# Kernel optimization log

Measured on AMD Instinct MI355X. Metric: run time of the kernel, lower is better.

## Reference

```python
import jax, jax.numpy as jnp
import numpy as np
from jax import lax

BS, T, D, H, FF, KS, L = 8, 1024, 512, 8, 2048, 5, 6
DK = D // H  # 64


def setup_inputs() -> dict:
    key = jax.random.key(0)
    ks_ = jax.random.split(key, 16)
    n = lambda i, shape, s=0.02: jax.random.normal(ks_[i], shape, jnp.float32) * s
    return dict(
        q_embed_data=n(0, (BS, T, D), 1.0),
        qa_embed_data=n(1, (BS, T, D), 1.0),
        pid_embed_data=n(2, (BS, T, T), 1.0),  # unused for emb_type='qid'
        conv_w=n(3, (D, D, KS)), conv_b=jnp.zeros((D,), jnp.float32),
        sqrt_beta=n(4, (1, 1, D), 1.0),
        sm_g=jnp.ones((D,), jnp.float32), sm_b=jnp.zeros((D,), jnp.float32),
        k_w=n(5, (L, D, D)), k_b=jnp.zeros((L, D), jnp.float32),
        v_w=n(6, (L, D, D)), v_b=jnp.zeros((L, D), jnp.float32),
        out_w=n(7, (L, D, D)), out_b=jnp.zeros((L, D), jnp.float32),
        gammas=n(8, (L, H, 1, 1), 0.1),
        ln1_g=jnp.ones((L, D), jnp.float32), ln1_b=jnp.zeros((L, D), jnp.float32),
        ff1_w=n(9, (L, D, FF)), ff1_b=jnp.zeros((L, FF), jnp.float32),
        ff2_w=n(10, (L, FF, D)), ff2_b=jnp.zeros((L, D), jnp.float32),
        ln2_g=jnp.ones((L, D), jnp.float32), ln2_b=jnp.zeros((L, D), jnp.float32),
    )


def _layernorm(x, g, b, eps):
    m = jnp.mean(x, axis=-1, keepdims=True)
    v = jnp.mean((x - m) ** 2, axis=-1, keepdims=True)
    return g * (x - m) / jnp.sqrt(v + eps) + b


def _smooth(x, conv_w, conv_b, sqrt_beta, g, b):
    # x: [B,T,D]. Causal Conv1d: left-pad KS-1, crop to length T.
    xt = jnp.transpose(x, (0, 2, 1))  # [B,D,T]
    trend = lax.conv_general_dilated(
        xt, conv_w, window_strides=(1,), padding=[(KS - 1, 0)],
        dimension_numbers=('NCH', 'OIH', 'NCH')) + conv_b[None, :, None]
    trend = jnp.transpose(trend, (0, 2, 1))  # [B,T,D]
    random = x - trend
    seq = trend + sqrt_beta ** 2 * random
    return _layernorm(seq + x, g, b, 1e-12)


def _decay_attention(q, k, v, mask, gamma_param, zero_pad):
    # q,k,v: [B,H,T,DK]; mask: [1,1,T,T] bool
    neg = jnp.float32(-1e32)
    scores = jnp.einsum('bhqd,bhkd->bhqk', q, k) / np.float32(np.sqrt(DK))
    # detached distance-effect computation (no_grad in torch)
    s_ = jax.nn.softmax(jnp.where(mask, scores, neg), axis=-1) * mask.astype(jnp.float32)
    distcum = jnp.cumsum(s_, axis=-1)
    disttot = jnp.sum(s_, axis=-1, keepdims=True)
    idx = jnp.arange(T, dtype=jnp.float32)
    pos = jnp.abs(idx[None, :] - idx[:, None])[None, None]  # |j - i|
    dist = jnp.sqrt(jnp.clip((disttot - distcum) * pos, 0.0, None))
    dist = lax.stop_gradient(dist)
    gamma = -jax.nn.softplus(gamma_param)[None]  # [1,H,1,1]
    total_effect = jnp.clip(jnp.exp(dist * gamma), 1e-5, 1e5)
    scores = jnp.where(mask, scores * total_effect, neg)
    scores = jax.nn.softmax(scores, axis=-1)
    if zero_pad:
        scores = scores.at[:, :, 0, :].set(0.0)
    return jnp.einsum('bhqk,bhkd->bhqd', scores, v)


def _tlayer(p, i, mtype, q_in, k_in, v_in, apply_pos, masks):
    mask = masks[mtype]
    def heads(x, W, b):
        return jnp.transpose((x @ W + b).reshape(BS, T, H, DK), (0, 2, 1, 3))
    # kq_same=True: q and k both use k_linear
    q = heads(q_in, p['k_w'][i], p['k_b'][i])
    k = heads(k_in, p['k_w'][i], p['k_b'][i])
    v = heads(v_in, p['v_w'][i], p['v_b'][i])
    out = _decay_attention(q, k, v, mask, p['gammas'][i], zero_pad=(mtype == 0))
    concat = jnp.transpose(out, (0, 2, 1, 3)).reshape(BS, T, D)
    q2 = concat @ p['out_w'][i] + p['out_b'][i]
    x = _layernorm(q_in + q2, p['ln1_g'][i], p['ln1_b'][i], 1e-5)
    if apply_pos:
        hdn = jax.nn.relu(x @ p['ff1_w'][i] + p['ff1_b'][i])
        x = _layernorm(x + hdn @ p['ff2_w'][i] + p['ff2_b'][i],
                       p['ln2_g'][i], p['ln2_b'][i], 1e-5)
    return x


def _forward(q_embed_data, qa_embed_data, pid_embed_data,
             conv_w, conv_b, sqrt_beta, sm_g, sm_b,
             k_w, k_b, v_w, v_b, out_w, out_b, gammas,
             ln1_g, ln1_b, ff1_w, ff1_b, ff2_w, ff2_b, ln2_g, ln2_b):
    p = dict(k_w=k_w, k_b=k_b, v_w=v_w, v_b=v_b, out_w=out_w, out_b=out_b,
             gammas=gammas, ln1_g=ln1_g, ln1_b=ln1_b, ff1_w=ff1_w, ff1_b=ff1_b,
             ff2_w=ff2_w, ff2_b=ff2_b, ln2_g=ln2_g, ln2_b=ln2_b)
    tri = jnp.tril(jnp.ones((T, T), bool))
    masks = {1: tri[None, None], 0: jnp.tril(jnp.ones((T, T), bool), -1)[None, None]}
    x = _smooth(q_embed_data, conv_w, conv_b, sqrt_beta, sm_g, sm_b)
    y = _smooth(qa_embed_data, conv_w, conv_b, sqrt_beta, sm_g, sm_b)
    # blocks_1: n_blocks=2 layers, mask=1, self-attn on y
    y = _tlayer(p, 0, 1, y, y, y, True, masks)
    y = _tlayer(p, 1, 1, y, y, y, True, masks)
    # blocks_2: 4 layers alternating (mask=1, no FFN) / (mask=0, values=y, FFN)
    x = _tlayer(p, 2, 1, x, x, x, False, masks)
    x = _tlayer(p, 3, 0, x, x, y, True, masks)
    x = _tlayer(p, 4, 1, x, x, x, False, masks)
    x = _tlayer(p, 5, 0, x, x, y, True, masks)
    return x


def reference(q_embed_data, qa_embed_data, pid_embed_data,
              conv_w, conv_b, sqrt_beta, sm_g, sm_b,
              k_w, k_b, v_w, v_b, out_w, out_b, gammas,
              ln1_g, ln1_b, ff1_w, ff1_b, ff2_w, ff2_b, ln2_g, ln2_b):
    return _forward(q_embed_data, qa_embed_data, pid_embed_data,
                    conv_w, conv_b, sqrt_beta, sm_g, sm_b,
                    k_w, k_b, v_w, v_b, out_w, out_b, gammas,
                    ln1_g, ln1_b, ff1_w, ff1_b, ff2_w, ff2_b, ln2_g, ln2_b)
```

## Files before the change

### kernel.cpp

```cpp
#include <hip/hip_runtime.h>
#include <math.h>

#define T_  1024
#define D_  512
#define H_  8
#define DK_ 64
#define FF_ 2048
#define BSZ 8
#define M_  (BSZ * T_)
#define TP_ (T_ + 4)

typedef unsigned short u16;
typedef unsigned int u32;
typedef __attribute__((ext_vector_type(8))) __bf16 bf16x8;
typedef __attribute__((ext_vector_type(4))) float f32x4;

__device__ __forceinline__ u16 f2bf(float f) {
    unsigned int u = __float_as_uint(f);
    u += 0x7fffu + ((u >> 16) & 1u);
    return (u16)(u >> 16);
}
__device__ __forceinline__ float bf2f(u16 b) {
    return __uint_as_float((unsigned int)b << 16);
}

__device__ __forceinline__ void gload16(const void* g, void* l) {
    __builtin_amdgcn_global_load_lds(
        (const __attribute__((address_space(1))) void*)g,
        (__attribute__((address_space(3))) void*)l, 16, 0, 0);
}

__global__ void __launch_bounds__(256) gemm_mfma(
    const u16* __restrict__ A, const u16* __restrict__ Bt,
    const float* __restrict__ bias, void* __restrict__ Cout,
    int N, int K, int mode)
{
    __shared__ __align__(16) u16 As[128 * 32];
    __shared__ __align__(16) u16 Bs[128 * 32];
    int tid = threadIdx.x;
    int wid = tid >> 6, lane = tid & 63;
    int quad = lane >> 4, mrow = lane & 15;
    int m0 = blockIdx.y * 128, n0 = blockIdx.x * 128;
    int wr = (wid >> 1) * 64, wc = (wid & 1) * 64;

    const u16* Ap = A + (size_t)(m0 + (tid >> 2)) * K + (tid & 3) * 8;
    const u16* Bp = Bt + (size_t)(n0 + (tid >> 2)) * K + (tid & 3) * 8;
    char* lA = (char*)As + wid * 1024;
    char* lB = (char*)Bs + wid * 1024;

    f32x4 acc[4][4] = {};
    for (int k0 = 0; k0 < K; k0 += 32) {
        __syncthreads();
        gload16(Ap + k0, lA);
        gload16(Ap + (size_t)64 * K + k0, lA + 4096);
        gload16(Bp + k0, lB);
        gload16(Bp + (size_t)64 * K + k0, lB + 4096);
        asm volatile("s_waitcnt vmcnt(0)" ::: "memory");
        __syncthreads();
        bf16x8 af[4], bf[4];
#pragma unroll
        for (int t = 0; t < 4; ++t) {
            af[t] = *(const bf16x8*)&As[(wr + t * 16 + mrow) * 32 + quad * 8];
            bf[t] = *(const bf16x8*)&Bs[(wc + t * 16 + mrow) * 32 + quad * 8];
        }
#pragma unroll
        for (int rt = 0; rt < 4; ++rt)
#pragma unroll
            for (int ct = 0; ct < 4; ++ct)
                acc[rt][ct] = __builtin_amdgcn_mfma_f32_16x16x32_bf16(
                    af[rt], bf[ct], acc[rt][ct], 0, 0, 0);
    }

#pragma unroll
    for (int ct = 0; ct < 4; ++ct) {
        int col = n0 + wc + ct * 16 + mrow;
        float bv = bias ? bias[col] : 0.f;
#pragma unroll
        for (int rt = 0; rt < 4; ++rt) {
            int rowb = m0 + wr + rt * 16 + quad * 4;
            if (mode == 0) {
                float* C = (float*)Cout;
#pragma unroll
                for (int e = 0; e < 4; ++e)
                    C[(size_t)(rowb + e) * N + col] = acc[rt][ct][e] + bv;
            } else if (mode == 1) {
                u16* C = (u16*)Cout;
#pragma unroll
                for (int e = 0; e < 4; ++e)
                    C[(size_t)(rowb + e) * N + col] = f2bf(fmaxf(acc[rt][ct][e] + bv, 0.f));
            } else {
                u16* C = (u16*)Cout;
#pragma unroll
                for (int e = 0; e < 4; ++e)
                    C[(size_t)(rowb + e) * N + col] = f2bf(acc[rt][ct][e] + bv);
            }
        }
    }
}

__global__ void __launch_bounds__(256) gemm64_mfma(
    const u16* __restrict__ A, const u16* __restrict__ Bt,
    const float* __restrict__ bias, void* __restrict__ Cout,
    int N, int K, int mode)
{
    __shared__ __align__(16) u16 As[64 * 32];
    __shared__ __align__(16) u16 Bs[64 * 32];
    int tid = threadIdx.x;
    int wid = tid >> 6, lane = tid & 63;
    int quad = lane >> 4, mrow = lane & 15;
    int m0 = blockIdx.y * 64, n0 = blockIdx.x * 64;
    int wc = wid * 16;

    const u16* Ap = A + (size_t)(m0 + (tid >> 2)) * K + (tid & 3) * 8;
    const u16* Bp = Bt + (size_t)(n0 + (tid >> 2)) * K + (tid & 3) * 8;
    char* lA = (char*)As + wid * 1024;
    char* lB = (char*)Bs + wid * 1024;

    f32x4 acc[4] = {};
    for (int k0 = 0; k0 < K; k0 += 32) {
        __syncthreads();
        gload16(Ap + k0, lA);
        gload16(Bp + k0, lB);
        asm volatile("s_waitcnt vmcnt(0)" ::: "memory");
        __syncthreads();
        bf16x8 af[4];
#pragma unroll
        for (int t = 0; t < 4; ++t)
            af[t] = *(const bf16x8*)&As[(t * 16 + mrow) * 32 + quad * 8];
        bf16x8 bf = *(const bf16x8*)&Bs[(wc + mrow) * 32 + quad * 8];
#pragma unroll
        for (int rt = 0; rt < 4; ++rt)
            acc[rt] = __builtin_amdgcn_mfma_f32_16x16x32_bf16(af[rt], bf, acc[rt], 0, 0, 0);
    }

    int col = n0 + wc + mrow;
    float bv = bias ? bias[col] : 0.f;
#pragma unroll
    for (int rt = 0; rt < 4; ++rt) {
        int rowb = m0 + rt * 16 + quad * 4;
        if (mode == 0) {
            float* C = (float*)Cout;
#pragma unroll
            for (int e = 0; e < 4; ++e)
                C[(size_t)(rowb + e) * N + col] = acc[rt][e] + bv;
        } else if (mode == 1) {
            u16* C = (u16*)Cout;
#pragma unroll
            for (int e = 0; e < 4; ++e)
                C[(size_t)(rowb + e) * N + col] = f2bf(fmaxf(acc[rt][e] + bv, 0.f));
        } else if (mode == 2) {
            u16* C = (u16*)Cout;
#pragma unroll
            for (int e = 0; e < 4; ++e)
                C[(size_t)(rowb + e) * N + col] = f2bf(acc[rt][e] + bv);
        } else {
            u16* C = (u16*)Cout;
            int h = col >> 6, dl = col & 63;
#pragma unroll
            for (int e = 0; e < 4; ++e) {
                int row = rowb + e;
                int b = row >> 10, t = row & (T_ - 1);
                C[(((size_t)(b * H_ + h) * DK_ + dl) << 10) + t] =
                    f2bf(acc[rt][e] + bv);
            }
        }
    }
}

__global__ void __launch_bounds__(256) conv64_mfma(
    const u16* __restrict__ Xp, const u16* __restrict__ W5t, float* __restrict__ C)
{
    __shared__ __align__(16) u16 As[64 * 32];
    __shared__ __align__(16) u16 Bs[64 * 32];
    int tid = threadIdx.x;
    int wid = tid >> 6, lane = tid & 63;
    int quad = lane >> 4, mrow = lane & 15;
    int m0 = blockIdx.y * 64, n0 = blockIdx.x * 64;
    int wc = wid * 16;
    int b = m0 >> 10, tloc = m0 & (T_ - 1);

    const u16* Ap0 = Xp + (size_t)(b * TP_ + tloc + (tid >> 2)) * D_ + (tid & 3) * 8;
    const u16* Bp0 = W5t + (size_t)(n0 + (tid >> 2)) * D_ + (tid & 3) * 8;
    char* lA = (char*)As + wid * 1024;
    char* lB = (char*)Bs + wid * 1024;

    f32x4 acc[4] = {};
    for (int ks = 0; ks < 5; ++ks) {
        const u16* Ap = Ap0 + ks * D_;
        const u16* Bp = Bp0 + (size_t)ks * D_ * D_;
        for (int k0 = 0; k0 < D_; k0 += 32) {
            __syncthreads();
            gload16(Ap + k0, lA);
            gload16(Bp + k0, lB);
            asm volatile("s_waitcnt vmcnt(0)" ::: "memory");
            __syncthreads();
            bf16x8 af[4];
#pragma unroll
            for (int t = 0; t < 4; ++t)
                af[t] = *(const bf16x8*)&As[(t * 16 + mrow) * 32 + quad * 8];
            bf16x8 bf = *(const bf16x8*)&Bs[(wc + mrow) * 32 + quad * 8];
#pragma unroll
            for (int rt = 0; rt < 4; ++rt)
                acc[rt] = __builtin_amdgcn_mfma_f32_16x16x32_bf16(af[rt], bf, acc[rt], 0, 0, 0);
        }
    }
    int col = n0 + wc + mrow;
#pragma unroll
    for (int rt = 0; rt < 4; ++rt) {
        int row = m0 + rt * 16 + quad * 4;
#pragma unroll
        for (int e = 0; e < 4; ++e)
            C[(size_t)(row + e) * D_ + col] = acc[rt][e];
    }
}

__global__ void __launch_bounds__(256) qk_mfma(
    const u16* __restrict__ Qh, u16* __restrict__ S)
{
    int kt = blockIdx.x, it = blockIdx.y;
    if (kt > it) return;
    int z = blockIdx.z;
    int b = z >> 3, h = z & 7;
    __shared__ __align__(16) u16 As[64 * 32];
    __shared__ __align__(16) u16 Bs[64 * 32];
    int tid = threadIdx.x;
    int wid = tid >> 6, lane = tid & 63;
    int quad = lane >> 4, mrow = lane & 15;
    int wc = wid * 16;

    const u16* Ap = Qh + (size_t)(b * T_ + it * 64 + (tid >> 2)) * D_ + h * DK_ + (tid & 3) * 8;
    const u16* Bp = Qh + (size_t)(b * T_ + kt * 64 + (tid >> 2)) * D_ + h * DK_ + (tid & 3) * 8;
    char* lA = (char*)As + wid * 1024;
    char* lB = (char*)Bs + wid * 1024;

    f32x4 acc[4] = {};
#pragma unroll
    for (int k0 = 0; k0 < DK_; k0 += 32) {
        __syncthreads();
        gload16(Ap + k0, lA);
        gload16(Bp + k0, lB);
        asm volatile("s_waitcnt vmcnt(0)" ::: "memory");
        __syncthreads();
        bf16x8 af[4];
#pragma unroll
        for (int t = 0; t < 4; ++t)
            af[t] = *(const bf16x8*)&As[(t * 16 + mrow) * 32 + quad * 8];
        bf16x8 bf = *(const bf16x8*)&Bs[(wc + mrow) * 32 + quad * 8];
#pragma unroll
        for (int rt = 0; rt < 4; ++rt)
            acc[rt] = __builtin_amdgcn_mfma_f32_16x16x32_bf16(af[rt], bf, acc[rt], 0, 0, 0);
    }
    int col = kt * 64 + wc + mrow;
#pragma unroll
    for (int rt = 0; rt < 4; ++rt) {
        int row = it * 64 + rt * 16 + quad * 4;
#pragma unroll
        for (int e = 0; e < 4; ++e)
            S[((size_t)z * T_ + row + e) * T_ + col] = f2bf(acc[rt][e] * 0.125f);
    }
}

#define LOG2E 1.4426950408889634f

#define DPPF(OLDB, X, CTRL, RM) \
    __uint_as_float((u32)__builtin_amdgcn_update_dpp( \
        (int)(OLDB), __float_as_int(X), CTRL, RM, 0xf, false))

__device__ __forceinline__ float scan_add_f(float x) {
    x += DPPF(0u, x, 0x111, 0xf);
    x += DPPF(0u, x, 0x112, 0xf);
    x += DPPF(0u, x, 0x114, 0xf);
    x += DPPF(0u, x, 0x118, 0xf);
    x += DPPF(0u, x, 0x142, 0xa);
    x += DPPF(0u, x, 0x143, 0xc);
    return x;
}
__device__ __forceinline__ float scan_max_f(float x) {
    x = fmaxf(x, DPPF(0xff800000u, x, 0x111, 0xf));
    x = fmaxf(x, DPPF(0xff800000u, x, 0x112, 0xf));
    x = fmaxf(x, DPPF(0xff800000u, x, 0x114, 0xf));
    x = fmaxf(x, DPPF(0xff800000u, x, 0x118, 0xf));
    x = fmaxf(x, DPPF(0xff800000u, x, 0x142, 0xa));
    x = fmaxf(x, DPPF(0xff800000u, x, 0x143, 0xc));
    return x;
}
__device__ __forceinline__ float lane63(float x) {
    return __uint_as_float((u32)__builtin_amdgcn_readlane(__float_as_int(x), 63));
}

__global__ void __launch_bounds__(256) decay_rows(
    u16* __restrict__ S, const float* __restrict__ gam_l, int mtype)
{
    int tid = threadIdx.x;
    int wv = tid >> 6, lane = tid & 63;
    int i = blockIdx.x * 4 + wv;
    int z = blockIdx.y;
    int h = z & 7;
    u16* row = S + ((size_t)z * T_ + i) * T_;
    int kmax = (mtype == 0) ? (i - 1) : i;

    if (kmax < 0) {
        row[lane] = 0;
        return;
    }
    int nc    = (kmax >> 7) + 1;
    int nfull = (kmax + 1) >> 7;
    int wend  = (((i >> 6) + 1) * 64 + 127) >> 7;

    float s0[8], s1[8], p0[8], p1[8];
    int base = lane * 2;

    float mx = -1e30f;
#pragma unroll
    for (int c = 0; c < 8; ++c) {
        if (c >= nc) break;
        int k = c * 128 + base;
        u32 v = *(const u32*)(row + k);
        float a = __uint_as_float(v << 16) * LOG2E;
        float b = __uint_as_float(v & 0xffff0000u) * LOG2E;
        if (c >= nfull) {
            a = (k     <= kmax) ? a : -1.5e30f;
            b = (k + 1 <= kmax) ? b : -1.5e30f;
        }
        s0[c] = a; s1[c] = b;
        mx = fmaxf(mx, fmaxf(a, b));
    }
    mx = lane63(scan_max_f(mx));

    float t1 = 0.f;
#pragma unroll
    for (int c = 0; c < 8; ++c) {
        if (c >= nc) break;
        float e0 = __builtin_amdgcn_exp2f(s0[c] - mx);
        float e1 = __builtin_amdgcn_exp2f(s1[c] - mx);
        p0[c] = e0; p1[c] = e1;
        t1 += e0 + e1;
    }
    float tot = lane63(scan_add_f(t1));
    float inv1 = 1.f / tot;

    float gam = -log1pf(__expf(gam_l[h])) * LOG2E;
    float fi = (float)i;
    float kf = (float)base;
    float running = 0.f;
#pragma unroll
    for (int c = 0; c < 8; ++c) {
        if (c >= nc) break;
        float sc = scan_add_f(p0[c] + p1[c]);
        float incl1 = running + sc;
        float incl0 = incl1 - p1[c];
        running += lane63(sc);
        float rem0 = fmaxf((tot - incl0) * inv1, 0.f);
        float rem1 = fmaxf((tot - incl1) * inv1, 0.f);
        float pos0 = fabsf(kf - fi);
        float pos1 = fabsf(kf + 1.f - fi);
        float ef0 = __builtin_amdgcn_fmed3f(
            __builtin_amdgcn_exp2f(sqrtf(rem0 * pos0) * gam), 1e-5f, 1e5f);
        float ef1 = __builtin_amdgcn_fmed3f(
            __builtin_amdgcn_exp2f(sqrtf(rem1 * pos1) * gam), 1e-5f, 1e5f);
        s0[c] *= ef0;
        s1[c] *= ef1;
        kf += 128.f;
    }

    float mx2 = -1e30f;
#pragma unroll
    for (int c = 0; c < 8; ++c) {
        if (c >= nc) break;
        mx2 = fmaxf(mx2, fmaxf(s0[c], s1[c]));
    }
    mx2 = lane63(scan_max_f(mx2));
    float t2 = 0.f;
#pragma unroll
    for (int c = 0; c < 8; ++c) {
        if (c >= nc) break;
        float e0 = __builtin_amdgcn_exp2f(s0[c] - mx2);
        float e1 = __builtin_amdgcn_exp2f(s1[c] - mx2);
        p0[c] = e0; p1[c] = e1;
        t2 += e0 + e1;
    }
    float tot2 = lane63(scan_add_f(t2));
    float inv2 = 1.f / tot2;

#pragma unroll
    for (int c = 0; c < 8; ++c) {
        if (c >= nc) break;
        float lo = p0[c] * inv2, hi = p1[c] * inv2;
        u32 o;
        asm("v_cvt_pk_bf16_f32 %0, %1, %2" : "=v"(o) : "v"(lo), "v"(hi));
        *(u32*)(row + c * 128 + base) = o;
    }
#pragma unroll
    for (int c = 0; c < 8; ++c) {
        if (c < nc) continue;
        if (c >= wend) break;
        *(u32*)(row + c * 128 + base) = 0u;
    }
}

__global__ void __launch_bounds__(256) pv_mfma(
    const u16* __restrict__ P, const u16* __restrict__ Vt,
    u16* __restrict__ O)
{
    int mt = blockIdx.x;
    int z = blockIdx.y;
    int b = z >> 3, h = z & 7;
    __shared__ __align__(16) u16 As[64 * 32];
    __shared__ __align__(16) u16 Bs[64 * 32];
    int tid = threadIdx.x;
    int wid = tid >> 6, lane = tid & 63;
    int quad = lane >> 4, mrow = lane & 15;
    int wc = wid * 16;

    const u16* Ap = P + ((size_t)z * T_ + mt * 64 + (tid >> 2)) * T_ + (tid & 3) * 8;
    const u16* Bp = Vt + ((size_t)z * DK_ + (tid >> 2)) * T_ + (tid & 3) * 8;
    char* lA = (char*)As + wid * 1024;
    char* lB = (char*)Bs + wid * 1024;

    int kend = (mt + 1) * 64;
    f32x4 acc[4] = {};
    for (int k0 = 0; k0 < kend; k0 += 32) {
        __syncthreads();
        gload16(Ap + k0, lA);
        gload16(Bp + k0, lB);
        asm volatile("s_waitcnt vmcnt(0)" ::: "memory");
        __syncthreads();
        bf16x8 af[4];
#pragma unroll
        for (int t = 0; t < 4; ++t)
            af[t] = *(const bf16x8*)&As[(t * 16 + mrow) * 32 + quad * 8];
        bf16x8 bf = *(const bf16x8*)&Bs[(wc + mrow) * 32 + quad * 8];
#pragma unroll
        for (int rt = 0; rt < 4; ++rt)
            acc[rt] = __builtin_amdgcn_mfma_f32_16x16x32_bf16(af[rt], bf, acc[rt], 0, 0, 0);
    }
    int col = h * DK_ + wc + mrow;
#pragma unroll
    for (int rt = 0; rt < 4; ++rt) {
        int row = b * T_ + mt * 64 + rt * 16 + quad * 4;
#pragma unroll
        for (int e = 0; e < 4; ++e)
            O[(size_t)(row + e) * D_ + col] = f2bf(acc[rt][e]);
    }
}

__global__ void __launch_bounds__(256) transpose_bf16(
    const float* __restrict__ W, u16* __restrict__ Wt, int K, int N)
{
    __shared__ float tile[32][33];
    size_t base = (size_t)blockIdx.z * K * N;
    W += base; Wt += base;
    int k0 = blockIdx.y * 32, n0 = blockIdx.x * 32;
    int r = threadIdx.x >> 3, c = (threadIdx.x & 7) * 4;
    float4 v = *(const float4*)(W + (size_t)(k0 + r) * N + n0 + c);
    tile[r][c] = v.x; tile[r][c + 1] = v.y; tile[r][c + 2] = v.z; tile[r][c + 3] = v.w;
    __syncthreads();
    ushort4 o;
    o.x = f2bf(tile[c + 0][r]); o.y = f2bf(tile[c + 1][r]);
    o.z = f2bf(tile[c + 2][r]); o.w = f2bf(tile[c + 3][r]);
    *(ushort4*)(Wt + (size_t)(n0 + r) * K + k0 + c) = o;
}

__global__ void w5_gather(const float* __restrict__ cw, u16* __restrict__ W5t)
{
    int idx = blockIdx.x * 256 + threadIdx.x;
    if (idx >= 5 * D_ * D_) return;
    int ks = idx / (D_ * D_);
    int rem = idx - ks * (D_ * D_);
    int o = rem >> 9, i = rem & (D_ - 1);
    W5t[idx] = f2bf(cw[((size_t)o * D_ + i) * 5 + ks]);
}

__global__ void cast_pad(const float* __restrict__ x, const float* __restrict__ y,
                         u16* __restrict__ Xp, u16* __restrict__ Yp)
{
    int idx = blockIdx.x * 256 + threadIdx.x;
    if (idx >= BSZ * TP_ * D_) return;
    int d = idx & (D_ - 1);
    int rowp = idx >> 9;
    int b = rowp / TP_;
    int t = rowp - b * TP_;
    u16 vx = 0, vy = 0;
    if (t >= 4) {
        size_t src = ((size_t)(b * T_ + t - 4) << 9) + d;
        vx = f2bf(x[src]); vy = f2bf(y[src]);
    }
    Xp[idx] = vx; Yp[idx] = vy;
}

__global__ void __launch_bounds__(256) smooth_ln(
    const float* __restrict__ x, const float* __restrict__ trend,
    const float* __restrict__ conv_b, const float* __restrict__ sqrt_beta,
    const float* __restrict__ g, const float* __restrict__ bb,
    float* __restrict__ out, u16* __restrict__ outb)
{
    __shared__ float s_red[8];
    int row = blockIdx.x, tid = threadIdx.x;
    int lane = tid & 63, wid = tid >> 6;
    float2 xv = ((const float2*)(x + (size_t)row * D_))[tid];
    float2 tv = ((const float2*)(trend + (size_t)row * D_))[tid];
    float2 cb = ((const float2*)conv_b)[tid];
    float2 sb = ((const float2*)sqrt_beta)[tid];
    float t0 = tv.x + cb.x, t1 = tv.y + cb.y;
    float v0 = t0 + sb.x * sb.x * (xv.x - t0) + xv.x;
    float v1 = t1 + sb.y * sb.y * (xv.y - t1) + xv.y;
    float s = v0 + v1, sq = v0 * v0 + v1 * v1;
    for (int o = 32; o > 0; o >>= 1) { s += __shfl_xor(s, o, 64); sq += __shfl_xor(sq, o, 64); }
    if (lane == 0) { s_red[wid] = s; s_red[4 + wid] = sq; }
    __syncthreads();
    s = s_red[0] + s_red[1] + s_red[2] + s_red[3];
    sq = s_red[4] + s_red[5] + s_red[6] + s_red[7];
    float mean = s * (1.f / D_);
    float var = sq * (1.f / D_) - mean * mean;
    if (var < 0.f) var = 0.f;
    float rstd = rsqrtf(var + 1e-12f);
    float2 gv = ((const float2*)g)[tid];
    float2 bv = ((const float2*)bb)[tid];
    float2 o2;
    o2.x = gv.x * (v0 - mean) * rstd + bv.x;
    o2.y = gv.y * (v1 - mean) * rstd + bv.y;
    ((float2*)(out + (size_t)row * D_))[tid] = o2;
    ushort2 ob; ob.x = f2bf(o2.x); ob.y = f2bf(o2.y);
    ((ushort2*)(outb + (size_t)row * D_))[tid] = ob;
}

__global__ void __launch_bounds__(256) add_ln(
    const float* __restrict__ a, const float* __restrict__ c,
    const float* __restrict__ g, const float* __restrict__ bb,
    float* __restrict__ out, u16* __restrict__ outb, float eps)
{
    __shared__ float s_red[8];
    int row = blockIdx.x, tid = threadIdx.x;
    int lane = tid & 63, wid = tid >> 6;
    float2 av = ((const float2*)(a + (size_t)row * D_))[tid];
    float2 cv = ((const float2*)(c + (size_t)row * D_))[tid];
    float v0 = av.x + cv.x;
    float v1 = av.y + cv.y;
    float s = v0 + v1, sq = v0 * v0 + v1 * v1;
    for (int o = 32; o > 0; o >>= 1) { s += __shfl_xor(s, o, 64); sq += __shfl_xor(sq, o, 64); }
    if (lane == 0) { s_red[wid] = s; s_red[4 + wid] = sq; }
    __syncthreads();
    s = s_red[0] + s_red[1] + s_red[2] + s_red[3];
    sq = s_red[4] + s_red[5] + s_red[6] + s_red[7];
    float mean = s * (1.f / D_);
    float var = sq * (1.f / D_) - mean * mean;
    if (var < 0.f) var = 0.f;
    float rstd = rsqrtf(var + eps);
    float2 gv = ((const float2*)g)[tid];
    float2 bv = ((const float2*)bb)[tid];
    float2 o2;
    o2.x = gv.x * (v0 - mean) * rstd + bv.x;
    o2.y = gv.y * (v1 - mean) * rstd + bv.y;
    ((float2*)(out + (size_t)row * D_))[tid] = o2;
    ushort2 ob; ob.x = f2bf(o2.x); ob.y = f2bf(o2.y);
    ((ushort2*)(outb + (size_t)row * D_))[tid] = ob;
}

extern "C" void kernel_launch(void* const* d_in, const int* in_sizes, int n_in,
                              void* d_out, int out_size, void* d_ws, size_t ws_size,
                              hipStream_t stream)
{
    const float* q_embed   = (const float*)d_in[0];
    const float* qa_embed  = (const float*)d_in[1];
    const float* conv_w    = (const float*)d_in[3];
    const float* conv_b    = (const float*)d_in[4];
    const float* sqrt_beta = (const float*)d_in[5];
    const float* sm_g      = (const float*)d_in[6];
    const float* sm_b      = (const float*)d_in[7];
    const float* k_w       = (const float*)d_in[8];
    const float* k_b       = (const float*)d_in[9];
    const float* v_w       = (const float*)d_in[10];
    const float* v_b       = (const float*)d_in[11];
    const float* out_w     = (const float*)d_in[12];
    const float* out_b     = (const float*)d_in[13];
    const float* gammas    = (const float*)d_in[14];
    const float* ln1_g     = (const float*)d_in[15];
    const float* ln1_b     = (const float*)d_in[16];
    const float* ff1_w     = (const float*)d_in[17];
    const float* ff1_b     = (const float*)d_in[18];
    const float* ff2_w     = (const float*)d_in[19];
    const float* ff2_b     = (const float*)d_in[20];
    const float* ln2_g     = (const float*)d_in[21];
    const float* ln2_b     = (const float*)d_in[22];

    const size_t NT = (size_t)M_ * D_;
    float* X = (float*)d_out;
    char* w = (char*)d_ws;
    float* Y  = (float*)w; w += NT * 4;
    float* Fb = (float*)w; w += NT * 4;
    u16* Sb = (u16*)w;
    u16* Hb = Sb;
    u16* Xpad = Sb;
    u16* Ypad = Xpad + (size_t)BSZ * TP_ * D_;
    u16* W5t  = Ypad + (size_t)BSZ * TP_ * D_;
    w += (size_t)BSZ * H_ * T_ * T_ * 2;
    u16* Xb  = (u16*)w; w += NT * 2;
    u16* Yb  = (u16*)w; w += NT * 2;
    u16* Cb  = (u16*)w; w += NT * 2;
    u16* Qh  = (u16*)w; w += NT * 2;
    u16* Vt  = (u16*)w; w += NT * 2;
    u16* KWt = (u16*)w; w += (size_t)6 * D_ * D_ * 2;
    u16* VWt = (u16*)w; w += (size_t)6 * D_ * D_ * 2;
    u16* OWt = (u16*)w; w += (size_t)6 * D_ * D_ * 2;
    u16* F1t = (u16*)w; w += (size_t)6 * D_ * FF_ * 2;
    u16* F2t = (u16*)w; w += (size_t)6 * FF_ * D_ * 2;

    dim3 blk(256);

    cast_pad<<<(BSZ * TP_ * D_ + 255) / 256, blk, 0, stream>>>(q_embed, qa_embed, Xpad, Ypad);
    w5_gather<<<(5 * D_ * D_ + 255) / 256, blk, 0, stream>>>(conv_w, W5t);
    transpose_bf16<<<dim3(D_ / 32, D_ / 32, 6), blk, 0, stream>>>(k_w, KWt, D_, D_);
    transpose_bf16<<<dim3(D_ / 32, D_ / 32, 6), blk, 0, stream>>>(v_w, VWt, D_, D_);
    transpose_bf16<<<dim3(D_ / 32, D_ / 32, 6), blk, 0, stream>>>(out_w, OWt, D_, D_);
    transpose_bf16<<<dim3(FF_ / 32, D_ / 32, 6), blk, 0, stream>>>(ff1_w, F1t, D_, FF_);
    transpose_bf16<<<dim3(D_ / 32, FF_ / 32, 6), blk, 0, stream>>>(ff2_w, F2t, FF_, D_);

    conv64_mfma<<<dim3(8, 128), blk, 0, stream>>>(Xpad, W5t, Fb);
    smooth_ln<<<M_, blk, 0, stream>>>(q_embed, Fb, conv_b, sqrt_beta, sm_g, sm_b, X, Xb);
    conv64_mfma<<<dim3(8, 128), blk, 0, stream>>>(Ypad, W5t, Fb);
    smooth_ln<<<M_, blk, 0, stream>>>(qa_embed, Fb, conv_b, sqrt_beta, sm_g, sm_b, Y, Yb);

    auto layer = [&](int l, int mtype, float* io, u16* iob, const u16* vinb, bool ffn) {
        gemm64_mfma<<<dim3(8, 128), blk, 0, stream>>>(iob, KWt + (size_t)l * D_ * D_,
                                                      k_b + (size_t)l * D_, Qh, D_, D_, 2);
        gemm64_mfma<<<dim3(8, 128), blk, 0, stream>>>(vinb, VWt + (size_t)l * D_ * D_,
                                                      v_b + (size_t)l * D_, Vt, D_, D_, 3);
        qk_mfma<<<dim3(16, 16, 64), blk, 0, stream>>>(Qh, Sb);
        decay_rows<<<dim3(T_ / 4, 64), blk, 0, stream>>>(Sb, gammas + l * H_, mtype);
        pv_mfma<<<dim3(16, 64), blk, 0, stream>>>(Sb, Vt, Cb);
        gemm64_mfma<<<dim3(8, 128), blk, 0, stream>>>(Cb, OWt + (size_t)l * D_ * D_,
                                                      out_b + (size_t)l * D_, Fb, D_, D_, 0);
        add_ln<<<M_, blk, 0, stream>>>(io, Fb, ln1_g + l * D_, ln1_b + l * D_, io, iob, 1e-5f);
        if (ffn) {
            gemm_mfma<<<dim3(16, 64), blk, 0, stream>>>(iob, F1t + (size_t)l * D_ * FF_,
                                                        ff1_b + (size_t)l * FF_, Hb, FF_, D_, 1);
            gemm64_mfma<<<dim3(8, 128), blk, 0, stream>>>(Hb, F2t + (size_t)l * FF_ * D_,
                                                          ff2_b + (size_t)l * D_, Fb, D_, FF_, 0);
            add_ln<<<M_, blk, 0, stream>>>(io, Fb, ln2_g + l * D_, ln2_b + l * D_, io, iob, 1e-5f);
        }
    };

    layer(0, 1, Y, Yb, Yb, true);
    layer(1, 1, Y, Yb, Yb, true);
    layer(2, 1, X, Xb, Xb, false);
    layer(3, 0, X, Xb, Yb, true);
    layer(4, 1, X, Xb, Xb, false);
    layer(5, 0, X, Xb, Yb, true);
}
```

Measured before the change: 1.804 ms.

## Double-buffer LDS tiles in all MFMA GEMM kernels to overlap loads

```diff
diff --git a/kernel.cpp b/kernel.cpp
--- a/kernel.cpp
+++ b/kernel.cpp
@@ -35,8 +35,8 @@
     const float* __restrict__ bias, void* __restrict__ Cout,
     int N, int K, int mode)
 {
-    __shared__ __align__(16) u16 As[128 * 32];
-    __shared__ __align__(16) u16 Bs[128 * 32];
+    __shared__ __align__(16) u16 As[2][128 * 32];
+    __shared__ __align__(16) u16 Bs[2][128 * 32];
     int tid = threadIdx.x;
     int wid = tid >> 6, lane = tid & 63;
     int quad = lane >> 4, mrow = lane & 15;
@@ -49,19 +49,27 @@
     char* lB = (char*)Bs + wid * 1024;
 
     f32x4 acc[4][4] = {};
+    gload16(Ap, lA);
+    gload16(Ap + (size_t)64 * K, lA + 4096);
+    gload16(Bp, lB);
+    gload16(Bp + (size_t)64 * K, lB + 4096);
+    __syncthreads();
+    int cur = 0;
     for (int k0 = 0; k0 < K; k0 += 32) {
-        __syncthreads();
-        gload16(Ap + k0, lA);
-        gload16(Ap + (size_t)64 * K + k0, lA + 4096);
-        gload16(Bp + k0, lB);
-        gload16(Bp + (size_t)64 * K + k0, lB + 4096);
-        asm volatile("s_waitcnt vmcnt(0)" ::: "memory");
-        __syncthreads();
+        int nxt = cur ^ 1;
+        if (k0 + 32 < K) {
+            gload16(Ap + k0 + 32, lA + nxt * 8192);
+            gload16(Ap + (size_t)64 * K + k0 + 32, lA + nxt * 8192 + 4096);
+            gload16(Bp + k0 + 32, lB + nxt * 8192);
+            gload16(Bp + (size_t)64 * K + k0 + 32, lB + nxt * 8192 + 4096);
+        }
+        const u16* as = As[cur];
+        const u16* bs = Bs[cur];
         bf16x8 af[4], bf[4];
 #pragma unroll
         for (int t = 0; t < 4; ++t) {
-            af[t] = *(const bf16x8*)&As[(wr + t * 16 + mrow) * 32 + quad * 8];
-            bf[t] = *(const bf16x8*)&Bs[(wc + t * 16 + mrow) * 32 + quad * 8];
+            af[t] = *(const bf16x8*)&as[(wr + t * 16 + mrow) * 32 + quad * 8];
+            bf[t] = *(const bf16x8*)&bs[(wc + t * 16 + mrow) * 32 + quad * 8];
         }
 #pragma unroll
         for (int rt = 0; rt < 4; ++rt)
@@ -69,6 +77,8 @@
             for (int ct = 0; ct < 4; ++ct)
                 acc[rt][ct] = __builtin_amdgcn_mfma_f32_16x16x32_bf16(
                     af[rt], bf[ct], acc[rt][ct], 0, 0, 0);
+        if (k0 + 32 < K) __syncthreads();
+        cur = nxt;
     }
 
 #pragma unroll
@@ -103,8 +113,8 @@
     const float* __restrict__ bias, void* __restrict__ Cout,
     int N, int K, int mode)
 {
-    __shared__ __align__(16) u16 As[64 * 32];
-    __shared__ __align__(16) u16 Bs[64 * 32];
+    __shared__ __align__(16) u16 As[2][64 * 32];
+    __shared__ __align__(16) u16 Bs[2][64 * 32];
     int tid = threadIdx.x;
     int wid = tid >> 6, lane = tid & 63;
     int quad = lane >> 4, mrow = lane & 15;
@@ -117,20 +127,28 @@
     char* lB = (char*)Bs + wid * 1024;
 
     f32x4 acc[4] = {};
+    gload16(Ap, lA);
+    gload16(Bp, lB);
+    __syncthreads();
+    int cur = 0;
     for (int k0 = 0; k0 < K; k0 += 32) {
-        __syncthreads();
-        gload16(Ap + k0, lA);
-        gload16(Bp + k0, lB);
-        asm volatile("s_waitcnt vmcnt(0)" ::: "memory");
-        __syncthreads();
+        int nxt = cur ^ 1;
+        if (k0 + 32 < K) {
+            gload16(Ap + k0 + 32, lA + nxt * 4096);
+            gload16(Bp + k0 + 32, lB + nxt * 4096);
+        }
+        const u16* as = As[cur];
+        const u16* bs = Bs[cur];
         bf16x8 af[4];
 #pragma unroll
         for (int t = 0; t < 4; ++t)
-            af[t] = *(const bf16x8*)&As[(t * 16 + mrow) * 32 + quad * 8];
-        bf16x8 bf = *(const bf16x8*)&Bs[(wc + mrow) * 32 + quad * 8];
+            af[t] = *(const bf16x8*)&as[(t * 16 + mrow) * 32 + quad * 8];
+        bf16x8 bf = *(const bf16x8*)&bs[(wc + mrow) * 32 + quad * 8];
 #pragma unroll
         for (int rt = 0; rt < 4; ++rt)
             acc[rt] = __builtin_amdgcn_mfma_f32_16x16x32_bf16(af[rt], bf, acc[rt], 0, 0, 0);
+        if (k0 + 32 < K) __syncthreads();
+        cur = nxt;
     }
 
     int col = n0 + wc + mrow;
@@ -170,8 +188,8 @@
 __global__ void __launch_bounds__(256) conv64_mfma(
     const u16* __restrict__ Xp, const u16* __restrict__ W5t, float* __restrict__ C)
 {
-    __shared__ __align__(16) u16 As[64 * 32];
-    __shared__ __align__(16) u16 Bs[64 * 32];
+    __shared__ __align__(16) u16 As[2][64 * 32];
+    __shared__ __align__(16) u16 Bs[2][64 * 32];
     int tid = threadIdx.x;
     int wid = tid >> 6, lane = tid & 63;
     int quad = lane >> 4, mrow = lane & 15;
@@ -185,24 +203,29 @@
     char* lB = (char*)Bs + wid * 1024;
 
     f32x4 acc[4] = {};
-    for (int ks = 0; ks < 5; ++ks) {
-        const u16* Ap = Ap0 + ks * D_;
-        const u16* Bp = Bp0 + (size_t)ks * D_ * D_;
-        for (int k0 = 0; k0 < D_; k0 += 32) {
-            __syncthreads();
-            gload16(Ap + k0, lA);
-            gload16(Bp + k0, lB);
-            asm volatile("s_waitcnt vmcnt(0)" ::: "memory");
-            __syncthreads();
-            bf16x8 af[4];
-#pragma unroll
-            for (int t = 0; t < 4; ++t)
-                af[t] = *(const bf16x8*)&As[(t * 16 + mrow) * 32 + quad * 8];
-            bf16x8 bf = *(const bf16x8*)&Bs[(wc + mrow) * 32 + quad * 8];
-#pragma unroll
-            for (int rt = 0; rt < 4; ++rt)
-                acc[rt] = __builtin_amdgcn_mfma_f32_16x16x32_bf16(af[rt], bf, acc[rt], 0, 0, 0);
-        }
+    gload16(Ap0, lA);
+    gload16(Bp0, lB);
+    __syncthreads();
+    int cur = 0;
+    for (int s = 0; s < 80; ++s) {
+        int nxt = cur ^ 1;
+        if (s + 1 < 80) {
+            int ks = (s + 1) >> 4, k0 = ((s + 1) & 15) * 32;
+            gload16(Ap0 + ks * D_ + k0, lA + nxt * 4096);
+            gload16(Bp0 + (size_t)ks * D_ * D_ + k0, lB + nxt * 4096);
+        }
+        const u16* as = As[cur];
+        const u16* bs = Bs[cur];
+        bf16x8 af[4];
+#pragma unroll
+        for (int t = 0; t < 4; ++t)
+            af[t] = *(const bf16x8*)&as[(t * 16 + mrow) * 32 + quad * 8];
+        bf16x8 bf = *(const bf16x8*)&bs[(wc + mrow) * 32 + quad * 8];
+#pragma unroll
+        for (int rt = 0; rt < 4; ++rt)
+            acc[rt] = __builtin_amdgcn_mfma_f32_16x16x32_bf16(af[rt], bf, acc[rt], 0, 0, 0);
+        if (s + 1 < 80) __syncthreads();
+        cur = nxt;
     }
     int col = n0 + wc + mrow;
 #pragma unroll
@@ -221,8 +244,8 @@
     if (kt > it) return;
     int z = blockIdx.z;
     int b = z >> 3, h = z & 7;
-    __shared__ __align__(16) u16 As[64 * 32];
-    __shared__ __align__(16) u16 Bs[64 * 32];
+    __shared__ __align__(16) u16 As[2][64 * 32];
+    __shared__ __align__(16) u16 Bs[2][64 * 32];
     int tid = threadIdx.x;
     int wid = tid >> 6, lane = tid & 63;
     int quad = lane >> 4, mrow = lane & 15;
@@ -233,19 +256,22 @@
     char* lA = (char*)As + wid * 1024;
     char* lB = (char*)Bs + wid * 1024;
 
+    gload16(Ap, lA);
+    gload16(Ap + 32, lA + 4096);
+    gload16(Bp, lB);
+    gload16(Bp + 32, lB + 4096);
+    __syncthreads();
+
     f32x4 acc[4] = {};
 #pragma unroll
-    for (int k0 = 0; k0 < DK_; k0 += 32) {
-        __syncthreads();
-        gload16(Ap + k0, lA);
-        gload16(Bp + k0, lB);
-        asm volatile("s_waitcnt vmcnt(0)" ::: "memory");
-        __syncthreads();
+    for (int s = 0; s < 2; ++s) {
+        const u16* as = As[s];
+        const u16* bs = Bs[s];
         bf16x8 af[4];
 #pragma unroll
         for (int t = 0; t < 4; ++t)
-            af[t] = *(const bf16x8*)&As[(t * 16 + mrow) * 32 + quad * 8];
-        bf16x8 bf = *(const bf16x8*)&Bs[(wc + mrow) * 32 + quad * 8];
+            af[t] = *(const bf16x8*)&as[(t * 16 + mrow) * 32 + quad * 8];
+        bf16x8 bf = *(const bf16x8*)&bs[(wc + mrow) * 32 + quad * 8];
 #pragma unroll
         for (int rt = 0; rt < 4; ++rt)
             acc[rt] = __builtin_amdgcn_mfma_f32_16x16x32_bf16(af[rt], bf, acc[rt], 0, 0, 0);
@@ -405,8 +431,8 @@
     int mt = blockIdx.x;
     int z = blockIdx.y;
     int b = z >> 3, h = z & 7;
-    __shared__ __align__(16) u16 As[64 * 32];
-    __shared__ __align__(16) u16 Bs[64 * 32];
+    __shared__ __align__(16) u16 As[2][64 * 32];
+    __shared__ __align__(16) u16 Bs[2][64 * 32];
     int tid = threadIdx.x;
     int wid = tid >> 6, lane = tid & 63;
     int quad = lane >> 4, mrow = lane & 15;
@@ -419,20 +445,28 @@
 
     int kend = (mt + 1) * 64;
     f32x4 acc[4] = {};
+    gload16(Ap, lA);
+    gload16(Bp, lB);
+    __syncthreads();
+    int cur = 0;
     for (int k0 = 0; k0 < kend; k0 += 32) {
-        __syncthreads();
-        gload16(Ap + k0, lA);
-        gload16(Bp + k0, lB);
-        asm volatile("s_waitcnt vmcnt(0)" ::: "memory");
-        __syncthreads();
+        int nxt = cur ^ 1;
+        if (k0 + 32 < kend) {
+            gload16(Ap + k0 + 32, lA + nxt * 4096);
+            gload16(Bp + k0 + 32, lB + nxt * 4096);
+        }
+        const u16* as = As[cur];
+        const u16* bs = Bs[cur];
         bf16x8 af[4];
 #pragma unroll
         for (int t = 0; t < 4; ++t)
-            af[t] = *(const bf16x8*)&As[(t * 16 + mrow) * 32 + quad * 8];
-        bf16x8 bf = *(const bf16x8*)&Bs[(wc + mrow) * 32 + quad * 8];
+            af[t] = *(const bf16x8*)&as[(t * 16 + mrow) * 32 + quad * 8];
+        bf16x8 bf = *(const bf16x8*)&bs[(wc + mrow) * 32 + quad * 8];
 #pragma unroll
         for (int rt = 0; rt < 4; ++rt)
             acc[rt] = __builtin_amdgcn_mfma_f32_16x16x32_bf16(af[rt], bf, acc[rt], 0, 0, 0);
+        if (k0 + 32 < kend) __syncthreads();
+        cur = nxt;
     }
     int col = h * DK_ + wc + mrow;
 #pragma unroll
```

Result: slower. 1.879 ms (+4.2%).

## Process each decay-attention row with a full 256-thread block instead of one wave

Applied to the files above, without the earlier changes.

```diff
diff --git a/kernel.cpp b/kernel.cpp
--- a/kernel.cpp
+++ b/kernel.cpp
@@ -293,108 +293,90 @@
 {
     int tid = threadIdx.x;
     int wv = tid >> 6, lane = tid & 63;
-    int i = blockIdx.x * 4 + wv;
+    int i = blockIdx.x;
     int z = blockIdx.y;
     int h = z & 7;
     u16* row = S + ((size_t)z * T_ + i) * T_;
     int kmax = (mtype == 0) ? (i - 1) : i;
 
     if (kmax < 0) {
-        row[lane] = 0;
+        if (tid < 32) ((u32*)row)[tid] = 0u;
         return;
     }
-    int nc    = (kmax >> 7) + 1;
-    int nfull = (kmax + 1) >> 7;
-    int wend  = (((i >> 6) + 1) * 64 + 127) >> 7;
-
-    float s0[8], s1[8], p0[8], p1[8];
-    int base = lane * 2;
-
-    float mx = -1e30f;
-#pragma unroll
-    for (int c = 0; c < 8; ++c) {
-        if (c >= nc) break;
-        int k = c * 128 + base;
-        u32 v = *(const u32*)(row + k);
-        float a = __uint_as_float(v << 16) * LOG2E;
-        float b = __uint_as_float(v & 0xffff0000u) * LOG2E;
-        if (c >= nfull) {
-            a = (k     <= kmax) ? a : -1.5e30f;
-            b = (k + 1 <= kmax) ? b : -1.5e30f;
-        }
-        s0[c] = a; s1[c] = b;
-        mx = fmaxf(mx, fmaxf(a, b));
-    }
-    mx = lane63(scan_max_f(mx));
-
-    float t1 = 0.f;
-#pragma unroll
-    for (int c = 0; c < 8; ++c) {
-        if (c >= nc) break;
-        float e0 = __builtin_amdgcn_exp2f(s0[c] - mx);
-        float e1 = __builtin_amdgcn_exp2f(s1[c] - mx);
-        p0[c] = e0; p1[c] = e1;
-        t1 += e0 + e1;
-    }
-    float tot = lane63(scan_add_f(t1));
+
+    __shared__ float l_mx[4], l_t1[4], l_sc[4], l_mx2[4], l_t2[4];
+
+    int k0 = tid * 4;
+    int kend_pv = ((i >> 6) + 1) * 64;
+
+    ushort4 v = *(const ushort4*)(row + k0);
+    float s0 = bf2f(v.x) * LOG2E, s1 = bf2f(v.y) * LOG2E;
+    float s2 = bf2f(v.z) * LOG2E, s3 = bf2f(v.w) * LOG2E;
+    if (k0     > kmax) s0 = -1.5e30f;
+    if (k0 + 1 > kmax) s1 = -1.5e30f;
+    if (k0 + 2 > kmax) s2 = -1.5e30f;
+    if (k0 + 3 > kmax) s3 = -1.5e30f;
+
+    float m4 = fmaxf(fmaxf(s0, s1), fmaxf(s2, s3));
+    float wm = scan_max_f(m4);
+    if (lane == 63) l_mx[wv] = wm;
+    __syncthreads();
+    float mx = fmaxf(fmaxf(l_mx[0], l_mx[1]), fmaxf(l_mx[2], l_mx[3]));
+
+    float p0 = __builtin_amdgcn_exp2f(s0 - mx);
+    float p1 = __builtin_amdgcn_exp2f(s1 - mx);
+    float p2 = __builtin_amdgcn_exp2f(s2 - mx);
+    float p3 = __builtin_amdgcn_exp2f(s3 - mx);
+    float t0 = p0, t1 = t0 + p1, t2 = t1 + p2, t3 = t2 + p3;
+    float sc = scan_add_f(t3);
+    if (lane == 63) l_sc[wv] = sc;
+    __syncthreads();
+    float tot  = l_sc[0] + l_sc[1] + l_sc[2] + l_sc[3];
+    float woff = (wv > 0 ? l_sc[0] : 0.f) + (wv > 1 ? l_sc[1] : 0.f)
+               + (wv > 2 ? l_sc[2] : 0.f);
+    float off = woff + sc - t3;
     float inv1 = 1.f / tot;
 
     float gam = -log1pf(__expf(gam_l[h])) * LOG2E;
     float fi = (float)i;
-    float kf = (float)base;
-    float running = 0.f;
-#pragma unroll
-    for (int c = 0; c < 8; ++c) {
-        if (c >= nc) break;
-        float sc = scan_add_f(p0[c] + p1[c]);
-        float incl1 = running + sc;
-        float incl0 = incl1 - p1[c];
-        running += lane63(sc);
-        float rem0 = fmaxf((tot - incl0) * inv1, 0.f);
-        float rem1 = fmaxf((tot - incl1) * inv1, 0.f);
-        float pos0 = fabsf(kf - fi);
-        float pos1 = fabsf(kf + 1.f - fi);
-        float ef0 = __builtin_amdgcn_fmed3f(
-            __builtin_amdgcn_exp2f(sqrtf(rem0 * pos0) * gam), 1e-5f, 1e5f);
-        float ef1 = __builtin_amdgcn_fmed3f(
-            __builtin_amdgcn_exp2f(sqrtf(rem1 * pos1) * gam), 1e-5f, 1e5f);
-        s0[c] *= ef0;
-        s1[c] *= ef1;
-        kf += 128.f;
-    }
-
-    float mx2 = -1e30f;
-#pragma unroll
-    for (int c = 0; c < 8; ++c) {
-        if (c >= nc) break;
-        mx2 = fmaxf(mx2, fmaxf(s0[c], s1[c]));
-    }
-    mx2 = lane63(scan_max_f(mx2));
-    float t2 = 0.f;
-#pragma unroll
-    for (int c = 0; c < 8; ++c) {
-        if (c >= nc) break;
-        float e0 = __builtin_amdgcn_exp2f(s0[c] - mx2);
-        float e1 = __builtin_amdgcn_exp2f(s1[c] - mx2);
-        p0[c] = e0; p1[c] = e1;
-        t2 += e0 + e1;
-    }
-    float tot2 = lane63(scan_add_f(t2));
+    float kf = (float)k0;
+#define EFFECT(sx, tx, kofs) do {                                           \
+        float incl = off + (tx);                                            \
+        float rem = fmaxf((tot - incl) * inv1, 0.f);                        \
+        float pos = fabsf(kf + (kofs) - fi);                                \
+        float ef = __builtin_amdgcn_fmed3f(                                 \
+            __builtin_amdgcn_exp2f(sqrtf(rem * pos) * gam), 1e-5f, 1e5f);   \
+        (sx) *= ef;                                                         \
+    } while (0)
+    EFFECT(s0, t0, 0.f);
+    EFFECT(s1, t1, 1.f);
+    EFFECT(s2, t2, 2.f);
+    EFFECT(s3, t3, 3.f);
+#undef EFFECT
+
+    m4 = fmaxf(fmaxf(s0, s1), fmaxf(s2, s3));
+    wm = scan_max_f(m4);
+    if (lane == 63) l_mx2[wv] = wm;
+    __syncthreads();
+    float mx2 = fmaxf(fmaxf(l_mx2[0], l_mx2[1]), fmaxf(l_mx2[2], l_mx2[3]));
+    p0 = __builtin_amdgcn_exp2f(s0 - mx2);
+    p1 = __builtin_amdgcn_exp2f(s1 - mx2);
+    p2 = __builtin_amdgcn_exp2f(s2 - mx2);
+    p3 = __builtin_amdgcn_exp2f(s3 - mx2);
+    float q4 = (p0 + p1) + (p2 + p3);
+    float ws = scan_add_f(q4);
+    if (lane == 63) l_t2[wv] = ws;
+    __syncthreads();
+    float tot2 = l_t2[0] + l_t2[1] + l_t2[2] + l_t2[3];
     float inv2 = 1.f / tot2;
 
-#pragma unroll
-    for (int c = 0; c < 8; ++c) {
-        if (c >= nc) break;
-        float lo = p0[c] * inv2, hi = p1[c] * inv2;
-        u32 o;
-        asm("v_cvt_pk_bf16_f32 %0, %1, %2" : "=v"(o) : "v"(lo), "v"(hi));
-        *(u32*)(row + c * 128 + base) = o;
-    }
-#pragma unroll
-    for (int c = 0; c < 8; ++c) {
-        if (c < nc) continue;
-        if (c >= wend) break;
-        *(u32*)(row + c * 128 + base) = 0u;
+    if (k0 < kend_pv) {
+        float a0 = p0 * inv2, a1 = p1 * inv2, a2 = p2 * inv2, a3 = p3 * inv2;
+        u32 o0, o1;
+        asm("v_cvt_pk_bf16_f32 %0, %1, %2" : "=v"(o0) : "v"(a0), "v"(a1));
+        asm("v_cvt_pk_bf16_f32 %0, %1, %2" : "=v"(o1) : "v"(a2), "v"(a3));
+        uint2 o; o.x = o0; o.y = o1;
+        *(uint2*)(row + k0) = o;
     }
 }
 
@@ -626,7 +608,7 @@
         gemm64_mfma<<<dim3(8, 128), blk, 0, stream>>>(vinb, VWt + (size_t)l * D_ * D_,
                                                       v_b + (size_t)l * D_, Vt, D_, D_, 3);
         qk_mfma<<<dim3(16, 16, 64), blk, 0, stream>>>(Qh, Sb);
-        decay_rows<<<dim3(T_ / 4, 64), blk, 0, stream>>>(Sb, gammas + l * H_, mtype);
+        decay_rows<<<dim3(T_, 64), blk, 0, stream>>>(Sb, gammas + l * H_, mtype);
         pv_mfma<<<dim3(16, 64), blk, 0, stream>>>(Sb, Vt, Cb);
         gemm64_mfma<<<dim3(8, 128), blk, 0, stream>>>(Cb, OWt + (size_t)l * D_ * D_,
                                                       out_b + (size_t)l * D_, Fb, D_, D_, 0);
```

After: 2.251 ms. 1.25x slower.
